# Optimization experiments

Measured on AMD Instinct MI355X. Metric: run time of the kernel, lower is better.

Reference implementation:

```python
import jax, jax.numpy as jnp
import numpy as np

N_QUBITS = 4
N_LAYERS = 3
LETTERS = "ijkl"  # one axis label per qubit; batch axis is 'b'
CNOT = np.array([[1, 0, 0, 0], [0, 1, 0, 0], [0, 0, 0, 1], [0, 0, 1, 0]], dtype=np.complex64).reshape(2, 2, 2, 2)


def _apply_1q(state, U, w, batched):
    # state: [B,2,2,2,2]; U: [2,2] (shared) or [B,2,2] (per-sample)
    s = "b" + LETTERS
    t = LETTERS[w]
    u = ("b" if batched else "") + "z" + t
    return jnp.einsum(f"{u},{s}->{s.replace(t, 'z')}", U, state)


def _apply_cnot(state, c, t):
    s = "b" + LETTERS
    a, b = LETTERS[c], LETTERS[t]
    out = s.replace(a, "x").replace(b, "y")
    return jnp.einsum(f"xy{a}{b},{s}->{out}", jnp.asarray(CNOT), state)


def _rx(theta):
    # theta: [B] -> batched RX gates [B,2,2]
    c = jnp.cos(theta / 2).astype(jnp.complex64)
    s = (-1j * jnp.sin(theta / 2)).astype(jnp.complex64)
    return jnp.stack([jnp.stack([c, s], -1), jnp.stack([s, c], -1)], -2)


def _rz(a):
    e = jnp.exp(-1j * a.astype(jnp.complex64) / 2)
    zero = jnp.zeros((), jnp.complex64)
    return jnp.array([[e, zero], [zero, jnp.conj(e)]])


def _ry(a):
    c = jnp.cos(a / 2).astype(jnp.complex64)
    s = jnp.sin(a / 2).astype(jnp.complex64)
    return jnp.array([[c, -s], [s, c]])


def _rot(phi, theta, omega):
    # PennyLane Rot = RZ(omega) @ RY(theta) @ RZ(phi)
    return _rz(omega) @ _ry(theta) @ _rz(phi)


def _circuit(qparams, z):
    # qparams: [n_layers, n_qubits, 3] float32; z: [B, n_qubits] float32
    B = z.shape[0]
    state = jnp.zeros((B,) + (2,) * N_QUBITS, jnp.complex64)
    state = state.at[:, 0, 0, 0, 0].set(1.0 + 0.0j)
    # data-encoding RX layer (per-sample angles -> batched gates)
    for w in range(N_QUBITS):
        state = _apply_1q(state, _rx(z[:, w]), w, batched=True)
    # variational layers: Rot on every wire then CNOT ladder
    for layer in range(N_LAYERS):
        for w in range(N_QUBITS):
            U = _rot(qparams[layer, w, 0], qparams[layer, w, 1], qparams[layer, w, 2])
            state = _apply_1q(state, U, w, batched=False)
        for w in range(N_QUBITS - 1):
            state = _apply_cnot(state, w, w + 1)
    probs = jnp.abs(state) ** 2  # [B,2,2,2,2] float32
    zsign = jnp.array([1.0, -1.0], jnp.float32)
    s = "b" + LETTERS
    evs = [jnp.einsum(f"{s},{LETTERS[w]}->b", probs, zsign) for w in range(N_QUBITS)]
    return jnp.stack(evs, axis=-1)  # [B, n_qubits]


def reference(x, enc_w, enc_b, qparams, cls_w, cls_b, bn_gamma, bn_beta):
    B = x.shape[0]
    # avg_pool2d(kernel_size=6) on 28x28 -> 4x4 (floor division drops last 4 rows/cols)
    pooled = x[:, :, :24, :24].reshape(B, 1, 4, 6, 4, 6).mean(axis=(3, 5)).reshape(B, 16)
    z = pooled @ enc_w.T + enc_b  # [B, n_qubits]
    evs = _circuit(qparams, z)    # [B, n_qubits]
    out = evs @ cls_w.T + cls_b   # [B, output_dim]
    # BatchNorm1d in training mode: biased batch statistics, eps=1e-5
    mu = out.mean(axis=0)
    var = ((out - mu) ** 2).mean(axis=0)
    out = (out - mu) / jnp.sqrt(var + 1e-5) * bn_gamma + bn_beta
    return out


def setup_inputs() -> dict:
    key = jax.random.key(0)
    ks = jax.random.split(key, 6)
    B = 32768
    return {
        "x": jax.random.normal(ks[0], (B, 1, 28, 28), jnp.float32),
        "enc_w": jax.random.normal(ks[1], (N_QUBITS, 16), jnp.float32) * 0.25,
        "enc_b": jnp.zeros((N_QUBITS,), jnp.float32),
        "qparams": jax.random.normal(ks[2], (N_LAYERS, N_QUBITS, 3), jnp.float32),
        "cls_w": jax.random.normal(ks[3], (4, N_QUBITS), jnp.float32) * 0.5,
        "cls_b": jnp.zeros((4,), jnp.float32),
        "bn_gamma": jnp.ones((4,), jnp.float32),
        "bn_beta": jnp.zeros((4,), jnp.float32),
    }
```

## Files before the change

### kernel.cpp

```cpp
#include <hip/hip_runtime.h>
#include <math.h>


#define BTOT 32768

__global__ __launch_bounds__(256) void fused_kernel(
    const float* __restrict__ x,
    const float* __restrict__ enc_w, const float* __restrict__ enc_b,
    const float* __restrict__ qparams,
    const float* __restrict__ cls_w, const float* __restrict__ cls_b,
    float* __restrict__ preBN, float* __restrict__ sums)
{
    __shared__ float sVrT[256];
    __shared__ float sViT[256];
    __shared__ float sW2[64];
    __shared__ float red[4][8];

    const int tid = threadIdx.x;

    if (tid < 64) {
        int j = tid >> 4, i = tid & 15;
        float acc = 0.f;
        #pragma unroll
        for (int w = 0; w < 4; ++w)
            acc += cls_w[j * 4 + w] * ((i & (8 >> w)) ? -1.f : 1.f);
        sW2[j * 16 + i] = acc;
    }
    if (tid < 16) {
        float pr[16], pi[16];
        #pragma unroll
        for (int i = 0; i < 16; ++i) { pr[i] = (i == tid) ? 1.f : 0.f; pi[i] = 0.f; }
        for (int layer = 0; layer < 3; ++layer) {
            for (int w = 0; w < 4; ++w) {
                const float* qp = qparams + (layer * 4 + w) * 3;
                float phi = qp[0], th = qp[1], om = qp[2];
                float c, s, ca, sa, cd, sd;
                sincosf(0.5f * th, &s, &c);
                sincosf(0.5f * (phi + om), &sa, &ca);
                sincosf(0.5f * (phi - om), &sd, &cd);
                float u00r =  c * ca, u00i = -c * sa;
                float u01r = -s * cd, u01i = -s * sd;
                float u10r =  s * cd, u10i = -s * sd;
                float u11r =  c * ca, u11i =  c * sa;
                int m = 8 >> w;
                for (int idx = 0; idx < 16; ++idx) {
                    if (idx & m) continue;
                    int i1 = idx | m;
                    float ar = pr[idx], ai = pi[idx], br = pr[i1], bi = pi[i1];
                    pr[idx] = u00r*ar - u00i*ai + u01r*br - u01i*bi;
                    pi[idx] = u00r*ai + u00i*ar + u01r*bi + u01i*br;
                    pr[i1]  = u10r*ar - u10i*ai + u11r*br - u11i*bi;
                    pi[i1]  = u10r*ai + u10i*ar + u11r*bi + u11i*br;
                }
            }
            for (int w = 0; w < 3; ++w) {
                int mc = 8 >> w, mt = 8 >> (w + 1);
                for (int idx = 0; idx < 16; ++idx) {
                    if ((idx & mc) && !(idx & mt)) {
                        int i1 = idx | mt;
                        float tr = pr[idx], ti = pi[idx];
                        pr[idx] = pr[i1]; pi[idx] = pi[i1];
                        pr[i1] = tr;      pi[i1] = ti;
                    }
                }
            }
        }
        int p = __popc(tid) & 3;
        #pragma unroll
        for (int i = 0; i < 16; ++i) {
            float re = pr[i], im = pi[i], vr, vi;
            if (p == 0)      { vr = re;  vi = im;  }
            else if (p == 1) { vr = im;  vi = -re; }
            else if (p == 2) { vr = -re; vi = -im; }
            else             { vr = -im; vi = re;  }
            sVrT[tid * 16 + i] = vr;
            sViT[tid * 16 + i] = vi;
        }
    }

    const int tg = blockIdx.x * 256 + tid;
    const int s  = tg >> 2, rg = tg & 3;
    const float* base = x + (size_t)s * 784 + rg * 6 * 28;
    float p0 = 0.f, p1 = 0.f, p2 = 0.f, p3 = 0.f;
    #pragma unroll
    for (int r = 0; r < 6; ++r) {
        const float4* rp = (const float4*)(base + r * 28);
        float4 v0 = rp[0], v1 = rp[1], v2 = rp[2], v3 = rp[3], v4 = rp[4], v5 = rp[5];
        p0 += (v0.x + v0.y) + (v0.z + v0.w) + (v1.x + v1.y);
        p1 += (v1.z + v1.w) + (v2.x + v2.y) + (v2.z + v2.w);
        p2 += (v3.x + v3.y) + (v3.z + v3.w) + (v4.x + v4.y);
        p3 += (v4.z + v4.w) + (v5.x + v5.y) + (v5.z + v5.w);
    }
    const float inv36 = 1.f / 36.f;
    float pv[4] = {p0 * inv36, p1 * inv36, p2 * inv36, p3 * inv36};

    float z[4];
    #pragma unroll
    for (int j = 0; j < 4; ++j) {
        float acc = 0.f;
        #pragma unroll
        for (int c = 0; c < 4; ++c) acc += enc_w[j * 16 + rg * 4 + c] * pv[c];
        z[j] = acc;
    }
    #pragma unroll
    for (int j = 0; j < 4; ++j) {
        z[j] += __shfl_xor(z[j], 1, 64);
        z[j] += __shfl_xor(z[j], 2, 64);
        z[j] += enc_b[j];
    }

    float cz[4], sz[4];
    #pragma unroll
    for (int j = 0; j < 4; ++j) sincosf(0.5f * z[j], &sz[j], &cz[j]);
    float a01[4] = {cz[0]*cz[1], cz[0]*sz[1], sz[0]*cz[1], sz[0]*sz[1]};
    float a23[4] = {cz[2]*cz[3], cz[2]*sz[3], sz[2]*cz[3], sz[2]*sz[3]};
    float rv[16];
    #pragma unroll
    for (int k = 0; k < 16; ++k) rv[k] = a01[k >> 2] * a23[k & 3];

    __syncthreads();

    float arA[4] = {0,0,0,0}, aiA[4] = {0,0,0,0};
    #pragma unroll
    for (int k = 0; k < 16; ++k) {
        float4 vr4 = *(const float4*)&sVrT[k * 16 + rg * 4];
        float4 vi4 = *(const float4*)&sViT[k * 16 + rg * 4];
        float rk = rv[k];
        arA[0] += vr4.x * rk; arA[1] += vr4.y * rk; arA[2] += vr4.z * rk; arA[3] += vr4.w * rk;
        aiA[0] += vi4.x * rk; aiA[1] += vi4.y * rk; aiA[2] += vi4.z * rk; aiA[3] += vi4.w * rk;
    }
    float out[4] = {0, 0, 0, 0};
    #pragma unroll
    for (int m = 0; m < 4; ++m) {
        float pp = arA[m] * arA[m] + aiA[m] * aiA[m];
        #pragma unroll
        for (int j = 0; j < 4; ++j) out[j] += sW2[j * 16 + rg * 4 + m] * pp;
    }
    #pragma unroll
    for (int j = 0; j < 4; ++j) {
        out[j] += __shfl_xor(out[j], 1, 64);
        out[j] += __shfl_xor(out[j], 2, 64);
        out[j] += cls_b[j];
    }
    if (rg == 0) ((float4*)preBN)[s] = make_float4(out[0], out[1], out[2], out[3]);

    float w = (rg == 0) ? 1.f : 0.f;
    float v8[8] = {out[0]*w, out[1]*w, out[2]*w, out[3]*w,
                   out[0]*out[0]*w, out[1]*out[1]*w, out[2]*out[2]*w, out[3]*out[3]*w};
    #pragma unroll
    for (int off = 32; off > 0; off >>= 1) {
        #pragma unroll
        for (int m = 0; m < 8; ++m) v8[m] += __shfl_down(v8[m], off, 64);
    }
    int wave = tid >> 6, lane = tid & 63;
    if (lane == 0) {
        #pragma unroll
        for (int m = 0; m < 8; ++m) red[wave][m] = v8[m];
    }
    __syncthreads();
    if (tid < 8)
        atomicAdd(&sums[tid], red[0][tid] + red[1][tid] + red[2][tid] + red[3][tid]);
}

__global__ __launch_bounds__(256) void bn_kernel(
    const float* __restrict__ sums,
    const float* __restrict__ gamma, const float* __restrict__ beta,
    float* __restrict__ out)
{
    int s = blockIdx.x * 256 + threadIdx.x;
    const float invB = 1.f / (float)BTOT;
    float4 v = ((const float4*)out)[s];
    float o[4] = {v.x, v.y, v.z, v.w};
    #pragma unroll
    for (int j = 0; j < 4; ++j) {
        float mu   = sums[j] * invB;
        float var  = sums[4 + j] * invB - mu * mu;
        float rstd = rsqrtf(var + 1e-5f);
        o[j] = (o[j] - mu) * rstd * gamma[j] + beta[j];
    }
    ((float4*)out)[s] = make_float4(o[0], o[1], o[2], o[3]);
}

extern "C" void kernel_launch(void* const* d_in, const int* in_sizes, int n_in,
                              void* d_out, int out_size, void* d_ws, size_t ws_size,
                              hipStream_t stream)
{
    const float* x        = (const float*)d_in[0];
    const float* enc_w    = (const float*)d_in[1];
    const float* enc_b    = (const float*)d_in[2];
    const float* qparams  = (const float*)d_in[3];
    const float* cls_w    = (const float*)d_in[4];
    const float* cls_b    = (const float*)d_in[5];
    const float* bn_gamma = (const float*)d_in[6];
    const float* bn_beta  = (const float*)d_in[7];

    float* sums = (float*)d_ws;
    float* outp = (float*)d_out;

    hipMemsetAsync(sums, 0, 8 * sizeof(float), stream);
    fused_kernel<<<512, 256, 0, stream>>>(x, enc_w, enc_b, qparams, cls_w, cls_b,
                                          outp, sums);
    bn_kernel<<<128, 256, 0, stream>>>(sums, bn_gamma, bn_beta, outp);
}
```

Measured before the change: 185.6 us.

## Stage pooled input rows in LDS with coalesced loads and use 16 threads per sample

Each block now cooperatively copies the first 24 rows of 16 samples into shared memory with contiguous float4 loads, then each of 16 threads per sample pools one 6x6 cell from LDS. Previously each of 4 threads per sample read strided rows straight from global memory. The per-sample work is remapped so each thread handles one basis state of the amplitude matrix-vector product, using padded LDS layouts to avoid bank conflicts. The change adds 43KB of LDS per block, which can reduce occupancy, and a block-wide barrier before compute. The launch grid grows to 2048 blocks, so the per-block 16-thread circuit precompute runs more often.

```diff
diff --git a/kernel.cpp b/kernel.cpp
--- a/kernel.cpp
+++ b/kernel.cpp
@@ -3,6 +3,8 @@
 
 
 #define BTOT 32768
+#define SPB  16
+#define SSTR 676
 
 __global__ __launch_bounds__(256) void fused_kernel(
     const float* __restrict__ x,
@@ -11,9 +13,10 @@
     const float* __restrict__ cls_w, const float* __restrict__ cls_b,
     float* __restrict__ preBN, float* __restrict__ sums)
 {
-    __shared__ float sVrT[256];
-    __shared__ float sViT[256];
-    __shared__ float sW2[64];
+    __shared__ float sx[SPB * SSTR];
+    __shared__ float sVr[16 * 17];
+    __shared__ float sVi[16 * 17];
+    __shared__ float sW2[4 * 17];
     __shared__ float red[4][8];
 
     const int tid = threadIdx.x;
@@ -24,7 +27,7 @@
         #pragma unroll
         for (int w = 0; w < 4; ++w)
             acc += cls_w[j * 4 + w] * ((i & (8 >> w)) ? -1.f : 1.f);
-        sW2[j * 16 + i] = acc;
+        sW2[j * 17 + i] = acc;
     }
     if (tid < 16) {
         float pr[16], pi[16];
@@ -73,41 +76,46 @@
             else if (p == 1) { vr = im;  vi = -re; }
             else if (p == 2) { vr = -re; vi = -im; }
             else             { vr = -im; vi = re;  }
-            sVrT[tid * 16 + i] = vr;
-            sViT[tid * 16 + i] = vi;
+            sVr[i * 17 + tid] = vr;
+            sVi[i * 17 + tid] = vi;
         }
     }
 
-    const int tg = blockIdx.x * 256 + tid;
-    const int s  = tg >> 2, rg = tg & 3;
-    const float* base = x + (size_t)s * 784 + rg * 6 * 28;
-    float p0 = 0.f, p1 = 0.f, p2 = 0.f, p3 = 0.f;
+    const int s0 = blockIdx.x * SPB;
+    const float4* xb = (const float4*)x;
+    #pragma unroll
+    for (int it = 0; it < 11; ++it) {
+        int gid = it * 256 + tid;
+        if (gid < SPB * 168) {
+            int c = gid / 168;
+            int o = gid - c * 168;
+            float4 v = xb[(size_t)(s0 + c) * 196 + o];
+            *(float4*)&sx[c * SSTR + o * 4] = v;
+        }
+    }
+    __syncthreads();
+
+    const int s = tid >> 4, cell = tid & 15;
+    const int cr = cell >> 2, cc = cell & 3;
+    const float* sb = &sx[s * SSTR + cr * 6 * 28 + cc * 6];
+    float sum = 0.f;
     #pragma unroll
     for (int r = 0; r < 6; ++r) {
-        const float4* rp = (const float4*)(base + r * 28);
-        float4 v0 = rp[0], v1 = rp[1], v2 = rp[2], v3 = rp[3], v4 = rp[4], v5 = rp[5];
-        p0 += (v0.x + v0.y) + (v0.z + v0.w) + (v1.x + v1.y);
-        p1 += (v1.z + v1.w) + (v2.x + v2.y) + (v2.z + v2.w);
-        p2 += (v3.x + v3.y) + (v3.z + v3.w) + (v4.x + v4.y);
-        p3 += (v4.z + v4.w) + (v5.x + v5.y) + (v5.z + v5.w);
-    }
-    const float inv36 = 1.f / 36.f;
-    float pv[4] = {p0 * inv36, p1 * inv36, p2 * inv36, p3 * inv36};
+        const float* rp = sb + r * 28;
+        sum += (rp[0] + rp[1]) + (rp[2] + rp[3]) + (rp[4] + rp[5]);
+    }
+    const float pv = sum * (1.f / 36.f);
 
     float z[4];
     #pragma unroll
-    for (int j = 0; j < 4; ++j) {
-        float acc = 0.f;
-        #pragma unroll
-        for (int c = 0; c < 4; ++c) acc += enc_w[j * 16 + rg * 4 + c] * pv[c];
-        z[j] = acc;
-    }
-    #pragma unroll
-    for (int j = 0; j < 4; ++j) {
-        z[j] += __shfl_xor(z[j], 1, 64);
-        z[j] += __shfl_xor(z[j], 2, 64);
-        z[j] += enc_b[j];
-    }
+    for (int j = 0; j < 4; ++j) z[j] = enc_w[j * 16 + cell] * pv;
+    #pragma unroll
+    for (int m = 1; m <= 8; m <<= 1) {
+        #pragma unroll
+        for (int j = 0; j < 4; ++j) z[j] += __shfl_xor(z[j], m, 64);
+    }
+    #pragma unroll
+    for (int j = 0; j < 4; ++j) z[j] += enc_b[j];
 
     float cz[4], sz[4];
     #pragma unroll
@@ -118,41 +126,36 @@
     #pragma unroll
     for (int k = 0; k < 16; ++k) rv[k] = a01[k >> 2] * a23[k & 3];
 
-    __syncthreads();
-
-    float arA[4] = {0,0,0,0}, aiA[4] = {0,0,0,0};
+    float ar = 0.f, ai = 0.f;
     #pragma unroll
     for (int k = 0; k < 16; ++k) {
-        float4 vr4 = *(const float4*)&sVrT[k * 16 + rg * 4];
-        float4 vi4 = *(const float4*)&sViT[k * 16 + rg * 4];
-        float rk = rv[k];
-        arA[0] += vr4.x * rk; arA[1] += vr4.y * rk; arA[2] += vr4.z * rk; arA[3] += vr4.w * rk;
-        aiA[0] += vi4.x * rk; aiA[1] += vi4.y * rk; aiA[2] += vi4.z * rk; aiA[3] += vi4.w * rk;
-    }
-    float out[4] = {0, 0, 0, 0};
-    #pragma unroll
-    for (int m = 0; m < 4; ++m) {
-        float pp = arA[m] * arA[m] + aiA[m] * aiA[m];
-        #pragma unroll
-        for (int j = 0; j < 4; ++j) out[j] += sW2[j * 16 + rg * 4 + m] * pp;
-    }
-    #pragma unroll
-    for (int j = 0; j < 4; ++j) {
-        out[j] += __shfl_xor(out[j], 1, 64);
-        out[j] += __shfl_xor(out[j], 2, 64);
-        out[j] += cls_b[j];
-    }
-    if (rg == 0) ((float4*)preBN)[s] = make_float4(out[0], out[1], out[2], out[3]);
-
-    float w = (rg == 0) ? 1.f : 0.f;
+        ar += sVr[cell * 17 + k] * rv[k];
+        ai += sVi[cell * 17 + k] * rv[k];
+    }
+    const float prob = ar * ar + ai * ai;
+    float out[4];
+    #pragma unroll
+    for (int j = 0; j < 4; ++j) out[j] = sW2[j * 17 + cell] * prob;
+    #pragma unroll
+    for (int m = 1; m <= 8; m <<= 1) {
+        #pragma unroll
+        for (int j = 0; j < 4; ++j) out[j] += __shfl_xor(out[j], m, 64);
+    }
+    #pragma unroll
+    for (int j = 0; j < 4; ++j) out[j] += cls_b[j];
+
+    if (cell == 0)
+        ((float4*)preBN)[s0 + s] = make_float4(out[0], out[1], out[2], out[3]);
+
+    const float w = (cell == 0) ? 1.f : 0.f;
     float v8[8] = {out[0]*w, out[1]*w, out[2]*w, out[3]*w,
                    out[0]*out[0]*w, out[1]*out[1]*w, out[2]*out[2]*w, out[3]*out[3]*w};
     #pragma unroll
-    for (int off = 32; off > 0; off >>= 1) {
-        #pragma unroll
-        for (int m = 0; m < 8; ++m) v8[m] += __shfl_down(v8[m], off, 64);
-    }
-    int wave = tid >> 6, lane = tid & 63;
+    for (int m = 0; m < 8; ++m) {
+        v8[m] += __shfl_down(v8[m], 32, 64);
+        v8[m] += __shfl_down(v8[m], 16, 64);
+    }
+    const int wave = tid >> 6, lane = tid & 63;
     if (lane == 0) {
         #pragma unroll
         for (int m = 0; m < 8; ++m) red[wave][m] = v8[m];
@@ -198,7 +201,7 @@
     float* outp = (float*)d_out;
 
     hipMemsetAsync(sums, 0, 8 * sizeof(float), stream);
-    fused_kernel<<<512, 256, 0, stream>>>(x, enc_w, enc_b, qparams, cls_w, cls_b,
-                                          outp, sums);
+    fused_kernel<<<BTOT / SPB, 256, 0, stream>>>(x, enc_w, enc_b, qparams,
+                                                 cls_w, cls_b, outp, sums);
     bn_kernel<<<128, 256, 0, stream>>>(sums, bn_gamma, bn_beta, outp);
 }
```

Measured after the change: 239.1 us. 28.8% more time.
